# Performance work log

Hardware: AMD Instinct MI355X
Metric: run time of the kernel (lower is better)

## Reference

```python
import jax, jax.numpy as jnp
import numpy as np

B, S, D_MODEL, H = 2, 2048, 1024, 16
HD = D_MODEL // H  # 64
THETA = 10000.0


def setup_inputs() -> dict:
    key = jax.random.key(0)
    ks = jax.random.split(key, 5)
    std = (2.0 / (D_MODEL + D_MODEL)) ** 0.5
    x = jax.random.normal(ks[0], (B, S, D_MODEL), dtype=jnp.float32)
    Wq = jax.random.normal(ks[1], (D_MODEL, D_MODEL), dtype=jnp.float32) * std
    Wk = jax.random.normal(ks[2], (D_MODEL, D_MODEL), dtype=jnp.float32) * std
    Wv = jax.random.normal(ks[3], (D_MODEL, D_MODEL), dtype=jnp.float32) * std
    Wo = jax.random.normal(ks[4], (D_MODEL, D_MODEL), dtype=jnp.float32) * std
    # RoPE tables (buffers)
    pos = jnp.arange(S, dtype=jnp.float32)
    freq = THETA ** (-jnp.arange(0, HD, 2, dtype=jnp.float32) / HD)  # [HD/2]
    ang = jnp.outer(pos, freq)  # [S, HD/2]
    token_positions = jnp.arange(S, dtype=jnp.int32)
    return {
        "x": x,
        "token_positions": token_positions,
        "use_rope": 1,
        "Wq": Wq, "Wk": Wk, "Wv": Wv, "Wo": Wo,
        "cos": jnp.cos(ang), "sin": jnp.sin(ang),
    }


def _apply_rope(t, c, sn):
    # t: [b,h,s,d]; c,sn: [s,d/2] (broadcast over b,h)
    e = t[..., 0::2]
    o = t[..., 1::2]
    return jnp.stack([e * c - o * sn, o * c + e * sn], axis=-1).reshape(t.shape)


def reference(x, token_positions, use_rope, Wq, Wk, Wv, Wo, cos, sin):
    b, s, _ = x.shape

    def split_heads(t):  # [b,s,D] -> [b,h,s,hd]
        return t.reshape(b, s, H, HD).transpose(0, 2, 1, 3)

    q = split_heads(x @ Wq.T)
    k = split_heads(x @ Wk.T)
    v = split_heads(x @ Wv.T)

    if use_rope:
        c = cos[token_positions]   # [s, hd/2]
        sn = sin[token_positions]  # [s, hd/2]
        q = _apply_rope(q, c, sn)
        k = _apply_rope(k, c, sn)

    scale = 1.0 / jnp.sqrt(jnp.float32(HD))
    scores = jnp.einsum('bhqd,bhkd->bhqk', q, k) * scale  # [b,h,s,s]
    causal = jnp.tril(jnp.ones((s, s), dtype=bool))
    scores = jnp.where(causal, scores, -jnp.inf)
    attn = jax.nn.softmax(scores, axis=-1)
    y = jnp.einsum('bhqk,bhkd->bhqd', attn, v)
    y = y.transpose(0, 2, 1, 3).reshape(b, s, D_MODEL)
    return y @ Wo.T
```

## Files before the change

### kernel.cpp

```cpp
#include <hip/hip_runtime.h>
#include <math.h>

#define BB 2
#define SS 2048
#define DM 1024
#define NH 16
#define HD 64

typedef __attribute__((ext_vector_type(8))) __bf16 bf16x8;
typedef __attribute__((ext_vector_type(4))) __bf16 bf16x4;
typedef __attribute__((ext_vector_type(8))) unsigned short u16x8;
typedef __attribute__((ext_vector_type(4))) float f32x4;
typedef unsigned short u16;
typedef unsigned int u32;
typedef __attribute__((address_space(1))) unsigned int u32g;
typedef __attribute__((address_space(3))) unsigned int u32l;

#define CEXP 0.18033688011112042f

static __device__ __forceinline__ u16 f2bf(float f) {
    __bf16 h = (__bf16)f;
    return __builtin_bit_cast(unsigned short, h);
}

static __device__ __forceinline__ void gld16(const u16* g, u16* l) {
    __builtin_amdgcn_global_load_lds((const u32g*)g, (u32l*)l, 16, 0, 0);
}

__global__ __launch_bounds__(256)
void cast_all(const float* __restrict__ x,
              const float* __restrict__ wq, const float* __restrict__ wk,
              const float* __restrict__ wv, const float* __restrict__ wo,
              u16* __restrict__ xb, u16* __restrict__ wqb, u16* __restrict__ wkb,
              u16* __restrict__ wvb, u16* __restrict__ wob)
{
    const int N4X = (BB * SS * DM) / 4;
    const int N4W = (DM * DM) / 4;
    int i = blockIdx.x * 256 + threadIdx.x;
    const float* src; u16* dst; int off;
    if (i < N4X) { src = x; dst = xb; off = i; }
    else {
        int i2 = i - N4X;
        int w = i2 >> 18;
        off = i2 & (N4W - 1);
        switch (w) {
            case 0:  src = wq; dst = wqb; break;
            case 1:  src = wk; dst = wkb; break;
            case 2:  src = wv; dst = wvb; break;
            default: src = wo; dst = wob; break;
        }
    }
    float4 v = ((const float4*)src)[off];
    ushort4 o;
    o.x = f2bf(v.x); o.y = f2bf(v.y); o.z = f2bf(v.z); o.w = f2bf(v.w);
    ((ushort4*)dst)[off] = o;
}

__global__ __launch_bounds__(256, 2)
void qkv_gemm(const u16* __restrict__ X,
              const u16* __restrict__ Wq, const u16* __restrict__ Wk,
              const u16* __restrict__ Wv,
              const int* __restrict__ tp, const float* __restrict__ cosp,
              const float* __restrict__ sinp, const int* __restrict__ use_rope,
              u16* __restrict__ Q, u16* __restrict__ K, u16* __restrict__ V)
{
    const u16* W; u16* dst;
    if (blockIdx.z == 0)      { W = Wq; dst = Q; }
    else if (blockIdx.z == 1) { W = Wk; dst = K; }
    else                      { W = Wv; dst = V; }

    __shared__ u16 As[128 * 64];
    __shared__ u16 Bs[128 * 64];
    const int t  = threadIdx.x;
    const int wv = t >> 6, L = t & 63, ln = L & 15, qd = L >> 4;
    const int i0 = blockIdx.y * 128, j0 = blockIdx.x * 128;
    const int wm = (wv >> 1) * 64, wn = (wv & 1) * 64;
    const int srow = L >> 3;
    const int scg  = ((L & 7) ^ (L >> 3)) * 8;

    f32x4 acc[4][4];
    #pragma unroll
    for (int a = 0; a < 4; ++a)
        #pragma unroll
        for (int b = 0; b < 4; ++b)
            #pragma unroll
            for (int e = 0; e < 4; ++e) acc[a][b][e] = 0.f;

    for (int k0 = 0; k0 < DM; k0 += 64) {
        __syncthreads();
        #pragma unroll
        for (int g = 0; g < 4; ++g) {
            int rb = wv * 32 + g * 8;
            gld16(X + (size_t)(i0 + rb + srow) * DM + k0 + scg, &As[rb * 64]);
            gld16(W + (size_t)(j0 + rb + srow) * DM + k0 + scg, &Bs[rb * 64]);
        }
        __syncthreads();
        bf16x8 a[4][2], b[4][2];
        #pragma unroll
        for (int mi = 0; mi < 4; ++mi)
            #pragma unroll
            for (int kd = 0; kd < 2; ++kd)
                a[mi][kd] = *(const bf16x8*)&As[(wm + mi * 16 + ln) * 64 + (((kd * 4 + qd) ^ (ln & 7)) * 8)];
        #pragma unroll
        for (int ni = 0; ni < 4; ++ni)
            #pragma unroll
            for (int kd = 0; kd < 2; ++kd)
                b[ni][kd] = *(const bf16x8*)&Bs[(wn + ni * 16 + ln) * 64 + (((kd * 4 + qd) ^ (ln & 7)) * 8)];
        #pragma unroll
        for (int kd = 0; kd < 2; ++kd)
            #pragma unroll
            for (int mi = 0; mi < 4; ++mi)
                #pragma unroll
                for (int ni = 0; ni < 4; ++ni)
                    acc[mi][ni] = __builtin_amdgcn_mfma_f32_16x16x32_bf16(a[mi][kd], b[ni][kd], acc[mi][ni], 0, 0, 0);
    }

    const int rope_on = (blockIdx.z < 2) ? use_rope[0] : 0;
    #pragma unroll
    for (int mi = 0; mi < 4; ++mi)
        #pragma unroll
        for (int r = 0; r < 4; ++r) {
            int gi = i0 + wm + mi * 16 + qd * 4 + r;
            int b_ = gi >> 11, s = gi & 2047;
            int pos = tp[s];
            #pragma unroll
            for (int ni = 0; ni < 4; ++ni) {
                int gj = j0 + wn + ni * 16 + ln;
                int h = gj >> 6, d = gj & 63;
                float v = acc[mi][ni][r];
                float pv = __shfl_xor(v, 1);
                if (rope_on) {
                    int p = d >> 1;
                    float c  = cosp[pos * 32 + p];
                    float sn = sinp[pos * 32 + p];
                    v = (d & 1) ? (v * c + pv * sn) : (v * c - pv * sn);
                }
                dst[(((size_t)(b_ * NH + h)) * SS + s) * HD + d] = f2bf(v);
            }
        }
}

__global__ __launch_bounds__(256, 2)
void out_gemm(const u16* __restrict__ X, const u16* __restrict__ W,
              float* __restrict__ dst)
{
    __shared__ u16 As[128 * 64];
    __shared__ u16 Bs[128 * 64];
    const int t  = threadIdx.x;
    const int wv = t >> 6, L = t & 63, ln = L & 15, qd = L >> 4;
    const int i0 = blockIdx.y * 128, j0 = blockIdx.x * 128;
    const int wm = (wv >> 1) * 64, wn = (wv & 1) * 64;
    const int srow = L >> 3;
    const int scg  = ((L & 7) ^ (L >> 3)) * 8;

    f32x4 acc[4][4];
    #pragma unroll
    for (int a = 0; a < 4; ++a)
        #pragma unroll
        for (int b = 0; b < 4; ++b)
            #pragma unroll
            for (int e = 0; e < 4; ++e) acc[a][b][e] = 0.f;

    for (int k0 = 0; k0 < DM; k0 += 64) {
        __syncthreads();
        #pragma unroll
        for (int g = 0; g < 4; ++g) {
            int rb = wv * 32 + g * 8;
            gld16(X + (size_t)(i0 + rb + srow) * DM + k0 + scg, &As[rb * 64]);
            gld16(W + (size_t)(j0 + rb + srow) * DM + k0 + scg, &Bs[rb * 64]);
        }
        __syncthreads();
        bf16x8 a[4][2], b[4][2];
        #pragma unroll
        for (int mi = 0; mi < 4; ++mi)
            #pragma unroll
            for (int kd = 0; kd < 2; ++kd)
                a[mi][kd] = *(const bf16x8*)&As[(wm + mi * 16 + ln) * 64 + (((kd * 4 + qd) ^ (ln & 7)) * 8)];
        #pragma unroll
        for (int ni = 0; ni < 4; ++ni)
            #pragma unroll
            for (int kd = 0; kd < 2; ++kd)
                b[ni][kd] = *(const bf16x8*)&Bs[(wn + ni * 16 + ln) * 64 + (((kd * 4 + qd) ^ (ln & 7)) * 8)];
        #pragma unroll
        for (int kd = 0; kd < 2; ++kd)
            #pragma unroll
            for (int mi = 0; mi < 4; ++mi)
                #pragma unroll
                for (int ni = 0; ni < 4; ++ni)
                    acc[mi][ni] = __builtin_amdgcn_mfma_f32_16x16x32_bf16(a[mi][kd], b[ni][kd], acc[mi][ni], 0, 0, 0);
    }

    #pragma unroll
    for (int mi = 0; mi < 4; ++mi)
        #pragma unroll
        for (int ni = 0; ni < 4; ++ni)
            #pragma unroll
            for (int r = 0; r < 4; ++r) {
                int gi = i0 + wm + mi * 16 + qd * 4 + r;
                int gj = j0 + wn + ni * 16 + ln;
                dst[(size_t)gi * DM + gj] = acc[mi][ni][r];
            }
}

static __device__ __forceinline__ void group_step(
    const bf16x8 af[4][2], const bf16x8 qf[2], u16* psw,
    int diag, int rowg, int j0, int ln, int qd,
    float& m, float& l, f32x4* o, bf16x8& pf0, bf16x8& pf1)
{
    f32x4 s[4];
    #pragma unroll
    for (int mt = 0; mt < 4; ++mt) {
        #pragma unroll
        for (int e = 0; e < 4; ++e) s[mt][e] = 0.f;
        s[mt] = __builtin_amdgcn_mfma_f32_16x16x32_bf16(af[mt][0], qf[0], s[mt], 0, 0, 0);
        s[mt] = __builtin_amdgcn_mfma_f32_16x16x32_bf16(af[mt][1], qf[1], s[mt], 0, 0, 0);
    }
    if (diag) {
        #pragma unroll
        for (int mt = 0; mt < 4; ++mt)
            #pragma unroll
            for (int r = 0; r < 4; ++r)
                if (j0 + mt * 16 + qd * 4 + r > rowg) s[mt][r] = -3.0e38f;
    }
    float rm = s[0][0];
    #pragma unroll
    for (int mt = 0; mt < 4; ++mt)
        #pragma unroll
        for (int r = 0; r < 4; ++r) rm = fmaxf(rm, s[mt][r]);
    rm = fmaxf(rm, __shfl_xor(rm, 16));
    rm = fmaxf(rm, __shfl_xor(rm, 32));
    float nm = fmaxf(m, rm);
    float alpha = exp2f((m - nm) * CEXP);
    float nmc = nm * CEXP;
    float rs = 0.f;
    #pragma unroll
    for (int mt = 0; mt < 4; ++mt) {
        bf16x4 pk;
        #pragma unroll
        for (int r = 0; r < 4; ++r) {
            float pv = exp2f(fmaf(s[mt][r], CEXP, -nmc));
            rs += pv;
            pk[r] = (__bf16)pv;
        }
        *(bf16x4*)(psw + ln * 72 + mt * 16 + qd * 4) = pk;
    }
    rs += __shfl_xor(rs, 16);
    rs += __shfl_xor(rs, 32);
    l = l * alpha + rs;
    m = nm;
    #pragma unroll
    for (int r = 0; r < 4; ++r) {
        float ar = __shfl(alpha, qd * 4 + r);
        #pragma unroll
        for (int ni = 0; ni < 4; ++ni) o[ni][r] *= ar;
    }
    pf0 = *(const bf16x8*)(psw + ln * 72 + qd * 8);
    pf1 = *(const bf16x8*)(psw + ln * 72 + 32 + qd * 8);
}

__global__ __launch_bounds__(256, 2)
void attn_kernel(const u16* __restrict__ Q, const u16* __restrict__ K,
                 const u16* __restrict__ V, u16* __restrict__ Y)
{
    __shared__ u16 Ks[64 * 64];
    __shared__ u16 Vt[64 * 64];
    __shared__ u16 Ps[4][2][16 * 72];

    const int t  = threadIdx.x;
    const int wv = t >> 6, L = t & 63, ln = L & 15, qd = L >> 4;
    const int bh = blockIdx.x, p = blockIdx.y;
    const int qbA = p * 64, qbB = (31 - p) * 64;
    const u16* Qp = Q + (size_t)bh * SS * HD;
    const u16* Kp = K + (size_t)bh * SS * HD;
    const u16* Vp = V + (size_t)bh * SS * HD;

    bf16x8 qfA[2], qfB[2];
    {
        const u16* ra = Qp + (size_t)(qbA + wv * 16 + ln) * HD;
        qfA[0] = *(const bf16x8*)(ra + qd * 8);
        qfA[1] = *(const bf16x8*)(ra + 32 + qd * 8);
        const u16* rb = Qp + (size_t)(qbB + wv * 16 + ln) * HD;
        qfB[0] = *(const bf16x8*)(rb + qd * 8);
        qfB[1] = *(const bf16x8*)(rb + 32 + qd * 8);
    }

    f32x4 oA[4], oB[4];
    #pragma unroll
    for (int ni = 0; ni < 4; ++ni)
        #pragma unroll
        for (int e = 0; e < 4; ++e) { oA[ni][e] = 0.f; oB[ni][e] = 0.f; }
    float mA = -3.0e38f, lA = 0.f, mB = -3.0e38f, lB = 0.f;

    const int ntile = 32 - p;
    for (int tix = 0; tix < ntile; ++tix) {
        const int j0 = tix * 64;
        __syncthreads();
        #pragma unroll
        for (int cc = 0; cc < 2; ++cc) {
            int c = t + cc * 256;
            int kr = c >> 3, c8 = c & 7;
            u16x8 val = *(const u16x8*)(Kp + (size_t)(j0 + kr) * HD + c8 * 8);
            *(u16x8*)&Ks[kr * 64 + ((c8 ^ (kr & 7)) * 8)] = val;
        }
        {
            int kp = t & 31, dg = t >> 5;
            const u16* v0 = Vp + (size_t)(j0 + 2 * kp) * HD + dg * 8;
            u16x8 va = *(const u16x8*)v0;
            u16x8 vb = *(const u16x8*)(v0 + HD);
            #pragma unroll
            for (int u = 0; u < 8; ++u) {
                int d = dg * 8 + u;
                u32 w = (u32)va[u] | ((u32)vb[u] << 16);
                *(u32*)&Vt[d * 64 + ((kp >> 2) ^ (d & 7)) * 8 + 2 * (kp & 3)] = w;
            }
        }
        __syncthreads();

        bf16x8 af[4][2];
        #pragma unroll
        for (int mt = 0; mt < 4; ++mt)
            #pragma unroll
            for (int kc = 0; kc < 2; ++kc)
                af[mt][kc] = *(const bf16x8*)&Ks[(mt * 16 + ln) * 64 + (((kc * 4 + qd) ^ (ln & 7)) * 8)];

        const bool hasA = (tix <= p);
        bf16x8 pA0, pA1, pB0, pB1;
        if (hasA)
            group_step(af, qfA, &Ps[wv][0][0], tix == p, qbA + wv * 16 + ln, j0, ln, qd,
                       mA, lA, oA, pA0, pA1);
        group_step(af, qfB, &Ps[wv][1][0], tix == ntile - 1, qbB + wv * 16 + ln, j0, ln, qd,
                   mB, lB, oB, pB0, pB1);

        #pragma unroll
        for (int kc = 0; kc < 2; ++kc)
            #pragma unroll
            for (int ni = 0; ni < 4; ++ni) {
                bf16x8 vf = *(const bf16x8*)&Vt[(ni * 16 + ln) * 64 + (((kc * 4 + qd) ^ (ln & 7)) * 8)];
                if (hasA)
                    oA[ni] = __builtin_amdgcn_mfma_f32_16x16x32_bf16(kc ? pA1 : pA0, vf, oA[ni], 0, 0, 0);
                oB[ni] = __builtin_amdgcn_mfma_f32_16x16x32_bf16(kc ? pB1 : pB0, vf, oB[ni], 0, 0, 0);
            }
    }

    const int b = bh >> 4, h = bh & 15;
    #pragma unroll
    for (int r = 0; r < 4; ++r) {
        float invA = 1.f / __shfl(lA, qd * 4 + r);
        float invB = 1.f / __shfl(lB, qd * 4 + r);
        int sA = qbA + wv * 16 + qd * 4 + r;
        int sB = qbB + wv * 16 + qd * 4 + r;
        #pragma unroll
        for (int ni = 0; ni < 4; ++ni) {
            int d = ni * 16 + ln;
            Y[((size_t)(b * SS + sA)) * DM + h * HD + d] = f2bf(oA[ni][r] * invA);
            Y[((size_t)(b * SS + sB)) * DM + h * HD + d] = f2bf(oB[ni][r] * invB);
        }
    }
}

extern "C" void kernel_launch(void* const* d_in, const int* in_sizes, int n_in,
                              void* d_out, int out_size, void* d_ws, size_t ws_size,
                              hipStream_t stream)
{
    const float* x        = (const float*)d_in[0];
    const int*   tp       = (const int*)d_in[1];
    const int*   use_rope = (const int*)d_in[2];
    const float* Wq       = (const float*)d_in[3];
    const float* Wk       = (const float*)d_in[4];
    const float* Wv       = (const float*)d_in[5];
    const float* Wo       = (const float*)d_in[6];
    const float* cosp     = (const float*)d_in[7];
    const float* sinp     = (const float*)d_in[8];
    float* out = (float*)d_out;

    char* ws = (char*)d_ws;
    const size_t MB = 1 << 20;
    u16* xb  = (u16*)(ws);
    u16* Wqb = (u16*)(ws + 8 * MB);
    u16* Wkb = (u16*)(ws + 10 * MB);
    u16* Wvb = (u16*)(ws + 12 * MB);
    u16* Wob = (u16*)(ws + 14 * MB);
    u16* Qb  = (u16*)(ws + 16 * MB);
    u16* Kb  = (u16*)(ws + 24 * MB);
    u16* Vb  = (u16*)(ws + 32 * MB);
    u16* Yb  = (u16*)(ws + 40 * MB);

    cast_all<<<8192, 256, 0, stream>>>(x, Wq, Wk, Wv, Wo, xb, Wqb, Wkb, Wvb, Wob);
    qkv_gemm<<<dim3(DM / 128, BB * SS / 128, 3), 256, 0, stream>>>(
        xb, Wqb, Wkb, Wvb, tp, cosp, sinp, use_rope, Qb, Kb, Vb);
    attn_kernel<<<dim3(BB * NH, 16), 256, 0, stream>>>(Qb, Kb, Vb, Yb);
    out_gemm<<<dim3(DM / 128, BB * SS / 128), 256, 0, stream>>>(Yb, Wob, out);
}
```

Baseline: 201.3 us.

## Stage GEMM epilogues through LDS, shrink out_gemm tile, use 128-key attention tiles

The QKV GEMM epilogue now stages the accumulators through shared memory and writes 16-byte coalesced rows, applying RoPE with vectorized cos/sin loads. Its launch bound is raised to 3 blocks per SM. The output GEMM switches to 128x64 tiles, doubling the grid, and writes through an LDS-staged coalesced float4 epilogue. The attention kernel processes 128 keys per tile, loads K asynchronously into LDS, and shares one P buffer per wave, cutting barriers and loop overhead. The cost is more registers and LDS pressure, plus a possible race from reusing the P buffer between the A and B steps.

```diff
diff --git a/kernel.cpp b/kernel.cpp
--- a/kernel.cpp
+++ b/kernel.cpp
@@ -21,6 +21,9 @@
 static __device__ __forceinline__ u16 f2bf(float f) {
     __bf16 h = (__bf16)f;
     return __builtin_bit_cast(unsigned short, h);
+}
+static __device__ __forceinline__ float bfu2f(u16 v) {
+    return __uint_as_float(((u32)v) << 16);
 }
 
 static __device__ __forceinline__ void gld16(const u16* g, u16* l) {
@@ -56,7 +59,7 @@
     ((ushort4*)dst)[off] = o;
 }
 
-__global__ __launch_bounds__(256, 2)
+__global__ __launch_bounds__(256, 3)
 void qkv_gemm(const u16* __restrict__ X,
               const u16* __restrict__ Wq, const u16* __restrict__ Wk,
               const u16* __restrict__ Wv,
@@ -69,8 +72,9 @@
     else if (blockIdx.z == 1) { W = Wk; dst = K; }
     else                      { W = Wv; dst = V; }
 
-    __shared__ u16 As[128 * 64];
-    __shared__ u16 Bs[128 * 64];
+    __shared__ u16 SH[4 * 64 * 68];
+    u16* As = SH;
+    u16* Bs = SH + 8192;
     const int t  = threadIdx.x;
     const int wv = t >> 6, L = t & 63, ln = L & 15, qd = L >> 4;
     const int i0 = blockIdx.y * 128, j0 = blockIdx.x * 128;
@@ -115,51 +119,63 @@
                     acc[mi][ni] = __builtin_amdgcn_mfma_f32_16x16x32_bf16(a[mi][kd], b[ni][kd], acc[mi][ni], 0, 0, 0);
     }
 
+    __syncthreads();
+    u16* Ts = SH + wv * (64 * 68);
+    #pragma unroll
+    for (int mi = 0; mi < 4; ++mi)
+        #pragma unroll
+        for (int ni = 0; ni < 4; ++ni)
+            #pragma unroll
+            for (int r = 0; r < 4; ++r)
+                Ts[(mi * 16 + qd * 4 + r) * 68 + ni * 16 + ln] = f2bf(acc[mi][ni][r]);
+
     const int rope_on = (blockIdx.z < 2) ? use_rope[0] : 0;
-    #pragma unroll
-    for (int mi = 0; mi < 4; ++mi)
-        #pragma unroll
-        for (int r = 0; r < 4; ++r) {
-            int gi = i0 + wm + mi * 16 + qd * 4 + r;
-            int b_ = gi >> 11, s = gi & 2047;
+    const int h  = blockIdx.x * 2 + (wv & 1);
+    const int sb = i0 + wm;
+    const int lrow = L >> 3, lcol = (L & 7) * 8;
+    #pragma unroll
+    for (int r2 = 0; r2 < 8; ++r2) {
+        int row = lrow + r2 * 8;
+        u16x8 val = *(const u16x8*)&Ts[row * 68 + lcol];
+        int sg = sb + row;
+        int b_ = sg >> 11, s = sg & 2047;
+        if (rope_on) {
             int pos = tp[s];
-            #pragma unroll
-            for (int ni = 0; ni < 4; ++ni) {
-                int gj = j0 + wn + ni * 16 + ln;
-                int h = gj >> 6, d = gj & 63;
-                float v = acc[mi][ni][r];
-                float pv = __shfl_xor(v, 1);
-                if (rope_on) {
-                    int p = d >> 1;
-                    float c  = cosp[pos * 32 + p];
-                    float sn = sinp[pos * 32 + p];
-                    v = (d & 1) ? (v * c + pv * sn) : (v * c - pv * sn);
-                }
-                dst[(((size_t)(b_ * NH + h)) * SS + s) * HD + d] = f2bf(v);
+            float cc[4], sc[4];
+            *(float4*)cc = *(const float4*)&cosp[pos * 32 + (lcol >> 1)];
+            *(float4*)sc = *(const float4*)&sinp[pos * 32 + (lcol >> 1)];
+            #pragma unroll
+            for (int j = 0; j < 4; ++j) {
+                float e = bfu2f(val[2 * j]), o = bfu2f(val[2 * j + 1]);
+                val[2 * j]     = f2bf(e * cc[j] - o * sc[j]);
+                val[2 * j + 1] = f2bf(o * cc[j] + e * sc[j]);
             }
         }
+        *(u16x8*)&dst[(((size_t)(b_ * NH + h)) * SS + s) * HD + lcol] = val;
+    }
 }
 
 __global__ __launch_bounds__(256, 2)
 void out_gemm(const u16* __restrict__ X, const u16* __restrict__ W,
               float* __restrict__ dst)
 {
-    __shared__ u16 As[128 * 64];
-    __shared__ u16 Bs[128 * 64];
+    __shared__ char SHB[36864];
+    u16* As = (u16*)SHB;
+    u16* Bs = (u16*)SHB + 8192;
     const int t  = threadIdx.x;
     const int wv = t >> 6, L = t & 63, ln = L & 15, qd = L >> 4;
-    const int i0 = blockIdx.y * 128, j0 = blockIdx.x * 128;
-    const int wm = (wv >> 1) * 64, wn = (wv & 1) * 64;
+    const int i0 = blockIdx.y * 128, j0 = blockIdx.x * 64;
+    const int wm = (wv >> 1) * 64, wn = (wv & 1) * 32;
     const int srow = L >> 3;
     const int scg  = ((L & 7) ^ (L >> 3)) * 8;
 
-    f32x4 acc[4][4];
-    #pragma unroll
-    for (int a = 0; a < 4; ++a)
-        #pragma unroll
-        for (int b = 0; b < 4; ++b)
-            #pragma unroll
-            for (int e = 0; e < 4; ++e) acc[a][b][e] = 0.f;
+    f32x4 acc[4][2];
+    #pragma unroll
+    for (int mi = 0; mi < 4; ++mi)
+        #pragma unroll
+        for (int ni = 0; ni < 2; ++ni)
+            #pragma unroll
+            for (int e = 0; e < 4; ++e) acc[mi][ni][e] = 0.f;
 
     for (int k0 = 0; k0 < DM; k0 += 64) {
         __syncthreads();
@@ -167,17 +183,21 @@
         for (int g = 0; g < 4; ++g) {
             int rb = wv * 32 + g * 8;
             gld16(X + (size_t)(i0 + rb + srow) * DM + k0 + scg, &As[rb * 64]);
+        }
+        #pragma unroll
+        for (int g = 0; g < 2; ++g) {
+            int rb = wv * 16 + g * 8;
             gld16(W + (size_t)(j0 + rb + srow) * DM + k0 + scg, &Bs[rb * 64]);
         }
         __syncthreads();
-        bf16x8 a[4][2], b[4][2];
+        bf16x8 a[4][2], b[2][2];
         #pragma unroll
         for (int mi = 0; mi < 4; ++mi)
             #pragma unroll
             for (int kd = 0; kd < 2; ++kd)
                 a[mi][kd] = *(const bf16x8*)&As[(wm + mi * 16 + ln) * 64 + (((kd * 4 + qd) ^ (ln & 7)) * 8)];
         #pragma unroll
-        for (int ni = 0; ni < 4; ++ni)
+        for (int ni = 0; ni < 2; ++ni)
             #pragma unroll
             for (int kd = 0; kd < 2; ++kd)
                 b[ni][kd] = *(const bf16x8*)&Bs[(wn + ni * 16 + ln) * 64 + (((kd * 4 + qd) ^ (ln & 7)) * 8)];
@@ -186,45 +206,54 @@
             #pragma unroll
             for (int mi = 0; mi < 4; ++mi)
                 #pragma unroll
-                for (int ni = 0; ni < 4; ++ni)
+                for (int ni = 0; ni < 2; ++ni)
                     acc[mi][ni] = __builtin_amdgcn_mfma_f32_16x16x32_bf16(a[mi][kd], b[ni][kd], acc[mi][ni], 0, 0, 0);
     }
 
+    __syncthreads();
+    float* Ts = (float*)SHB + wv * (64 * 36);
     #pragma unroll
     for (int mi = 0; mi < 4; ++mi)
         #pragma unroll
-        for (int ni = 0; ni < 4; ++ni)
-            #pragma unroll
-            for (int r = 0; r < 4; ++r) {
-                int gi = i0 + wm + mi * 16 + qd * 4 + r;
-                int gj = j0 + wn + ni * 16 + ln;
-                dst[(size_t)gi * DM + gj] = acc[mi][ni][r];
-            }
-}
-
-static __device__ __forceinline__ void group_step(
-    const bf16x8 af[4][2], const bf16x8 qf[2], u16* psw,
-    int diag, int rowg, int j0, int ln, int qd,
-    float& m, float& l, f32x4* o, bf16x8& pf0, bf16x8& pf1)
-{
-    f32x4 s[4];
-    #pragma unroll
-    for (int mt = 0; mt < 4; ++mt) {
+        for (int ni = 0; ni < 2; ++ni)
+            #pragma unroll
+            for (int r = 0; r < 4; ++r)
+                Ts[(mi * 16 + qd * 4 + r) * 36 + ni * 16 + ln] = acc[mi][ni][r];
+
+    const int lrow = L >> 3, lch = L & 7;
+    #pragma unroll
+    for (int r2 = 0; r2 < 8; ++r2) {
+        int row = lrow + r2 * 8;
+        float4 v = *(const float4*)&Ts[row * 36 + lch * 4];
+        *(float4*)&dst[(size_t)(i0 + wm + row) * DM + j0 + wn + lch * 4] = v;
+    }
+}
+
+static __device__ __forceinline__ void step128(
+    const u16* KsB, const bf16x8 qf[2], u16* psw,
+    bool mask, int rowg, int j0, int ln, int qd,
+    float& m, float& l, f32x4* o, bf16x8 pf[4])
+{
+    f32x4 s[8];
+    #pragma unroll
+    for (int mt = 0; mt < 8; ++mt) {
+        bf16x8 a0 = *(const bf16x8*)&KsB[(mt * 16 + ln) * 64 + ((qd ^ (ln & 7)) * 8)];
+        bf16x8 a1 = *(const bf16x8*)&KsB[(mt * 16 + ln) * 64 + (((4 + qd) ^ (ln & 7)) * 8)];
         #pragma unroll
         for (int e = 0; e < 4; ++e) s[mt][e] = 0.f;
-        s[mt] = __builtin_amdgcn_mfma_f32_16x16x32_bf16(af[mt][0], qf[0], s[mt], 0, 0, 0);
-        s[mt] = __builtin_amdgcn_mfma_f32_16x16x32_bf16(af[mt][1], qf[1], s[mt], 0, 0, 0);
-    }
-    if (diag) {
-        #pragma unroll
-        for (int mt = 0; mt < 4; ++mt)
+        s[mt] = __builtin_amdgcn_mfma_f32_16x16x32_bf16(a0, qf[0], s[mt], 0, 0, 0);
+        s[mt] = __builtin_amdgcn_mfma_f32_16x16x32_bf16(a1, qf[1], s[mt], 0, 0, 0);
+    }
+    if (mask) {
+        #pragma unroll
+        for (int mt = 0; mt < 8; ++mt)
             #pragma unroll
             for (int r = 0; r < 4; ++r)
                 if (j0 + mt * 16 + qd * 4 + r > rowg) s[mt][r] = -3.0e38f;
     }
     float rm = s[0][0];
     #pragma unroll
-    for (int mt = 0; mt < 4; ++mt)
+    for (int mt = 0; mt < 8; ++mt)
         #pragma unroll
         for (int r = 0; r < 4; ++r) rm = fmaxf(rm, s[mt][r]);
     rm = fmaxf(rm, __shfl_xor(rm, 16));
@@ -234,7 +263,7 @@
     float nmc = nm * CEXP;
     float rs = 0.f;
     #pragma unroll
-    for (int mt = 0; mt < 4; ++mt) {
+    for (int mt = 0; mt < 8; ++mt) {
         bf16x4 pk;
         #pragma unroll
         for (int r = 0; r < 4; ++r) {
@@ -242,7 +271,7 @@
             rs += pv;
             pk[r] = (__bf16)pv;
         }
-        *(bf16x4*)(psw + ln * 72 + mt * 16 + qd * 4) = pk;
+        *(bf16x4*)(psw + ln * 136 + mt * 16 + qd * 4) = pk;
     }
     rs += __shfl_xor(rs, 16);
     rs += __shfl_xor(rs, 32);
@@ -254,25 +283,32 @@
         #pragma unroll
         for (int ni = 0; ni < 4; ++ni) o[ni][r] *= ar;
     }
-    pf0 = *(const bf16x8*)(psw + ln * 72 + qd * 8);
-    pf1 = *(const bf16x8*)(psw + ln * 72 + 32 + qd * 8);
+    #pragma unroll
+    for (int kc = 0; kc < 4; ++kc)
+        pf[kc] = *(const bf16x8*)(psw + ln * 136 + kc * 32 + qd * 8);
 }
 
 __global__ __launch_bounds__(256, 2)
 void attn_kernel(const u16* __restrict__ Q, const u16* __restrict__ K,
                  const u16* __restrict__ V, u16* __restrict__ Y)
 {
-    __shared__ u16 Ks[64 * 64];
-    __shared__ u16 Vt[64 * 64];
-    __shared__ u16 Ps[4][2][16 * 72];
+    __shared__ u16 Ks[128 * 64];
+    __shared__ u16 Vt[64 * 128];
+    __shared__ u16 Ps[4][16 * 136];
 
     const int t  = threadIdx.x;
     const int wv = t >> 6, L = t & 63, ln = L & 15, qd = L >> 4;
     const int bh = blockIdx.x, p = blockIdx.y;
     const int qbA = p * 64, qbB = (31 - p) * 64;
+    const int cA = (p >> 1) + 1;
+    const int ntile = (33 - p) >> 1;
     const u16* Qp = Q + (size_t)bh * SS * HD;
     const u16* Kp = K + (size_t)bh * SS * HD;
     const u16* Vp = V + (size_t)bh * SS * HD;
+    const int srow = L >> 3;
+    const int scg  = ((L & 7) ^ (L >> 3)) * 8;
+    const int vkp = t & 63;
+    const int vdg0 = t >> 6;
 
     bf16x8 qfA[2], qfB[2];
     {
@@ -291,54 +327,45 @@
         for (int e = 0; e < 4; ++e) { oA[ni][e] = 0.f; oB[ni][e] = 0.f; }
     float mA = -3.0e38f, lA = 0.f, mB = -3.0e38f, lB = 0.f;
 
-    const int ntile = 32 - p;
     for (int tix = 0; tix < ntile; ++tix) {
-        const int j0 = tix * 64;
-        __syncthreads();
-        #pragma unroll
-        for (int cc = 0; cc < 2; ++cc) {
-            int c = t + cc * 256;
-            int kr = c >> 3, c8 = c & 7;
-            u16x8 val = *(const u16x8*)(Kp + (size_t)(j0 + kr) * HD + c8 * 8);
-            *(u16x8*)&Ks[kr * 64 + ((c8 ^ (kr & 7)) * 8)] = val;
-        }
-        {
-            int kp = t & 31, dg = t >> 5;
-            const u16* v0 = Vp + (size_t)(j0 + 2 * kp) * HD + dg * 8;
+        const int j0 = tix * 128;
+        __syncthreads();
+        #pragma unroll
+        for (int g = 0; g < 4; ++g) {
+            int rb = wv * 32 + g * 8;
+            gld16(Kp + (size_t)(j0 + rb + srow) * HD + scg, &Ks[rb * 64]);
+        }
+        #pragma unroll
+        for (int vvp = 0; vvp < 2; ++vvp) {
+            int dg = vdg0 + 4 * vvp;
+            const u16* v0 = Vp + (size_t)(j0 + 2 * vkp) * HD + dg * 8;
             u16x8 va = *(const u16x8*)v0;
             u16x8 vb = *(const u16x8*)(v0 + HD);
             #pragma unroll
             for (int u = 0; u < 8; ++u) {
                 int d = dg * 8 + u;
                 u32 w = (u32)va[u] | ((u32)vb[u] << 16);
-                *(u32*)&Vt[d * 64 + ((kp >> 2) ^ (d & 7)) * 8 + 2 * (kp & 3)] = w;
+                *(u32*)&Vt[d * 128 + (((vkp >> 2) ^ (d & 7)) * 8) + 2 * (vkp & 3)] = w;
             }
         }
         __syncthreads();
 
-        bf16x8 af[4][2];
-        #pragma unroll
-        for (int mt = 0; mt < 4; ++mt)
-            #pragma unroll
-            for (int kc = 0; kc < 2; ++kc)
-                af[mt][kc] = *(const bf16x8*)&Ks[(mt * 16 + ln) * 64 + (((kc * 4 + qd) ^ (ln & 7)) * 8)];
-
-        const bool hasA = (tix <= p);
-        bf16x8 pA0, pA1, pB0, pB1;
+        const bool hasA = (tix < cA);
+        bf16x8 pA[4], pB[4];
         if (hasA)
-            group_step(af, qfA, &Ps[wv][0][0], tix == p, qbA + wv * 16 + ln, j0, ln, qd,
-                       mA, lA, oA, pA0, pA1);
-        group_step(af, qfB, &Ps[wv][1][0], tix == ntile - 1, qbB + wv * 16 + ln, j0, ln, qd,
-                   mB, lB, oB, pB0, pB1);
-
-        #pragma unroll
-        for (int kc = 0; kc < 2; ++kc)
+            step128(Ks, qfA, &Ps[wv][0], tix == cA - 1, qbA + wv * 16 + ln, j0, ln, qd,
+                    mA, lA, oA, pA);
+        step128(Ks, qfB, &Ps[wv][0], tix == ntile - 1, qbB + wv * 16 + ln, j0, ln, qd,
+                mB, lB, oB, pB);
+
+        #pragma unroll
+        for (int kc = 0; kc < 4; ++kc)
             #pragma unroll
             for (int ni = 0; ni < 4; ++ni) {
-                bf16x8 vf = *(const bf16x8*)&Vt[(ni * 16 + ln) * 64 + (((kc * 4 + qd) ^ (ln & 7)) * 8)];
+                bf16x8 vf = *(const bf16x8*)&Vt[(ni * 16 + ln) * 128 + (((kc * 4 + qd) ^ (ln & 7)) * 8)];
                 if (hasA)
-                    oA[ni] = __builtin_amdgcn_mfma_f32_16x16x32_bf16(kc ? pA1 : pA0, vf, oA[ni], 0, 0, 0);
-                oB[ni] = __builtin_amdgcn_mfma_f32_16x16x32_bf16(kc ? pB1 : pB0, vf, oB[ni], 0, 0, 0);
+                    oA[ni] = __builtin_amdgcn_mfma_f32_16x16x32_bf16(pA[kc], vf, oA[ni], 0, 0, 0);
+                oB[ni] = __builtin_amdgcn_mfma_f32_16x16x32_bf16(pB[kc], vf, oB[ni], 0, 0, 0);
             }
     }
 
@@ -389,5 +416,5 @@
     qkv_gemm<<<dim3(DM / 128, BB * SS / 128, 3), 256, 0, stream>>>(
         xb, Wqb, Wkb, Wvb, tp, cosp, sinp, use_rope, Qb, Kb, Vb);
     attn_kernel<<<dim3(BB * NH, 16), 256, 0, stream>>>(Qb, Kb, Vb, Yb);
-    out_gemm<<<dim3(DM / 128, BB * SS / 128), 256, 0, stream>>>(Yb, Wob, out);
-}
+    out_gemm<<<dim3(DM / 64, BB * SS / 128), 256, 0, stream>>>(Yb, Wob, out);
+}
```

Result: faster. 196.4 us (-2.4%).
